# Kernel optimization log

Hardware: AMD Instinct MI355X
Metric: run time of the kernel (lower is better)

The kernel has to match this reference:

```python
import jax, jax.numpy as jnp
import numpy as np

HEADS = 16
SEGS = 8


def _rotate_half(x):
    x1, x2 = jnp.split(x, 2, axis=-1)
    return jnp.concatenate([-x2, x1], axis=-1)


def _split_heads(t, h):
    b, n, dim = t.shape
    d = dim // h
    return t.reshape(b, n, h, d).transpose(0, 2, 1, 3).reshape(b * h, n, d)


def _merge_heads(t, b, h):
    c, n, d = t.shape
    return t.reshape(b, h, n, d).transpose(0, 2, 1, 3).reshape(b, n, h * d)


def setup_inputs() -> dict:
    key = jax.random.key(0)
    ks = jax.random.split(key, 5)
    b, n, dim = 2, 4096, 1024
    x = jax.random.normal(ks[0], (b, n, dim), dtype=jnp.float32)
    w = lambda k: jax.random.normal(k, (dim, dim), dtype=jnp.float32) * 0.02
    return {
        'x': x,
        'Wq': w(ks[1]),
        'Wkv': w(ks[2]),
        'Wo': w(ks[3]),
        'bo': jnp.zeros((dim,), jnp.float32),
        'Wo0': w(ks[4]),
        'bo0': jnp.zeros((dim,), jnp.float32),
    }


def reference(x, Wq, Wkv, Wo, bo, Wo0, bo0):
    b, n, dim = x.shape
    h = HEADS
    d = dim // h
    s = SEGS
    m = n // s  # segment_len
    mask_value = -jnp.finfo(x.dtype).max

    q = _split_heads(x @ Wq, h)    # (b*h, n, d)
    kv = _split_heads(x @ Wkv, h)  # (b*h, n, d)  (serves as both keys and values)

    # rotary embedding (layer_num == 0 branch)
    inv_freq = 1.0 / (10000.0 ** (jnp.arange(0, d, 2, dtype=jnp.float32) / d))
    freqs = jnp.arange(n, dtype=jnp.float32)[:, None] * inv_freq[None, :]  # (n, d/2)
    rot = jnp.concatenate([freqs, freqs], axis=-1)[None]  # (1, n, d)
    cos, sin = jnp.cos(rot), jnp.sin(rot)
    q = q * cos + _rotate_half(q) * sin
    kv = kv * cos + _rotate_half(kv) * sin

    q = q * (d ** -0.5)

    qs = q.reshape(-1, s, m, d)   # (c, s, m, d)
    kvs = kv.reshape(-1, s, m, d)

    # overlapping windows: segment t paired with segment t+1 as kv context
    kvs_ccs = jnp.concatenate([kvs[:, :-1], kvs[:, 1:]], axis=2)  # (c, s-1, 2m, d)
    qs_ccs = qs[:, 1:]                                            # (c, s-1, m, d)

    # NOTE: original computes lkv = LayerNorm(kvs_ccs) but never uses it (dead code) -> omitted.

    lsim = jnp.einsum('csmd,csnd->csmn', qs_ccs, kvs_ccs)  # (c, s-1, m, 2m)
    causal = jnp.triu(jnp.ones((m, m), dtype=bool), 1)
    # causal mask only applied to second half of keys (the own segment t+1)
    lsim = jnp.concatenate(
        [lsim[..., :m], jnp.where(causal, mask_value, lsim[..., m:])], axis=-1)

    attn0 = jnp.einsum('csmd,csnd->csmn', qs[:, :1], kvs[:, :1])  # (c, 1, m, m)
    attn0 = jnp.where(causal, mask_value, attn0)

    attn0 = jax.nn.softmax(attn0, axis=-1)
    attn1 = jax.nn.softmax(lsim, axis=-1)

    out0 = jnp.einsum('csij,csjd->csid', attn0, kvs[:, :1]).reshape(-1, m, d)
    out1 = jnp.einsum('csij,csjd->csid', attn1, kvs_ccs).reshape(-1, (s - 1) * m, d)

    out0 = _merge_heads(out0, b, h) @ Wo0 + bo0  # (b, m, dim)
    out1 = _merge_heads(out1, b, h) @ Wo + bo    # (b, (s-1)*m, dim)
    return jnp.concatenate([out0, out1], axis=1)  # (b, n, dim)
```

## Files before the change

kernel.cpp:

```cpp
#include <hip/hip_runtime.h>
#include <hip/hip_bf16.h>
#include <float.h>

using bf16 = __hip_bfloat16;
typedef __attribute__((ext_vector_type(8))) short bf16x8;
typedef __attribute__((ext_vector_type(4))) float f32x4;
typedef __attribute__((ext_vector_type(16))) float f32x16;

#define DIM   1024
#define NSEQ  4096
#define BATCH 2
#define NH    16
#define HD    64
#define NSEG  8
#define MSEG  512
#define ROWS  (BATCH*NSEQ)
#define NC    (BATCH*NH)
#define QSCALE (0.125f * 1.44269504f)

__device__ __forceinline__ float fast_exp2(float x) {
    float r;
    asm volatile("v_exp_f32 %0, %1" : "=v"(r) : "v"(x));
    return r;
}

__device__ __forceinline__ void gload16(const bf16* g, bf16* l) {
    __builtin_amdgcn_global_load_lds((const __attribute__((address_space(1))) unsigned int*)g,
                                     (__attribute__((address_space(3))) unsigned int*)l, 16, 0, 0);
}

__global__ void k_rope_tab(float* __restrict__ cosT, float* __restrict__ sinT) {
    int idx = blockIdx.x * 256 + threadIdx.x;
    int t = idx >> 5, i = idx & 31;
    float freq = 1.0f / powf(10000.0f, (float)(2 * i) * (1.0f / 64.0f));
    float a = (float)t * freq;
    cosT[idx] = cosf(a);
    sinT[idx] = sinf(a);
}

__global__ void k_convert_x(const float* __restrict__ X, bf16* __restrict__ Xb) {
    int i = (blockIdx.x * 256 + threadIdx.x) * 4;
    float4 v = *(const float4*)&X[i];
    union { bf16 h[4]; uint2 u; } p;
    p.h[0] = __float2bfloat16(v.x);
    p.h[1] = __float2bfloat16(v.y);
    p.h[2] = __float2bfloat16(v.z);
    p.h[3] = __float2bfloat16(v.w);
    *(uint2*)&Xb[i] = p.u;
}

__global__ void k_transpose(const float* __restrict__ W, bf16* __restrict__ Wt) {
    __shared__ float tile[32][33];
    int bx = blockIdx.x * 32;
    int by = blockIdx.y * 32;
    int tx = threadIdx.x;
    for (int i = threadIdx.y; i < 32; i += 8)
        tile[i][tx] = W[(size_t)(by + i) * DIM + bx + tx];
    __syncthreads();
    for (int i = threadIdx.y; i < 32; i += 8)
        Wt[(size_t)(bx + i) * DIM + by + tx] = __float2bfloat16(tile[tx][i]);
}

__launch_bounds__(256, 4)
__global__ void k_gemm_qkv(const bf16* __restrict__ A, const bf16* __restrict__ Bq,
                           const bf16* __restrict__ Bkv, const float* __restrict__ cosT,
                           const float* __restrict__ sinT, bf16* __restrict__ Qb,
                           bf16* __restrict__ KVf) {
    __shared__ alignas(16) bf16 SH[18432];
    bf16* AsB = SH;
    bf16* BsB = SH + 8192;
    const int K = DIM;
    int tid = threadIdx.x;
    int lane = tid & 63, wave = tid >> 6;
    int hi = lane >> 5, lq = lane & 31;
    int wr = (wave >> 1) * 64, wc = (wave & 1) * 64;
    int id = blockIdx.x;
    int xcd = id & 7, rank = id >> 3;
    int by = xcd * 8 + (rank >> 4);
    int bxx = rank & 15;
    int m0 = by * 128;
    bool isQ = (bxx < 8);
    const bf16* Bt = isQ ? Bq : Bkv;
    int n0 = (bxx & 7) * 128;
    int row = lane & 15, kk = (lane >> 4) * 8;
    int ch0 = wave * 128 + lane, ch1 = ch0 + 64;
    int r0 = ch0 >> 2, c0e = (ch0 & 3) * 8;
    int r1 = ch1 >> 2, c1e = (ch1 & 3) * 8;
    f32x4 acc[4][4] = {};
    gload16(&A[(size_t)(m0 + r0) * K + c0e], &AsB[wave * 1024]);
    gload16(&A[(size_t)(m0 + r1) * K + c1e], &AsB[wave * 1024 + 512]);
    gload16(&Bt[(size_t)(n0 + r0) * K + c0e], &BsB[wave * 1024]);
    gload16(&Bt[(size_t)(n0 + r1) * K + c1e], &BsB[wave * 1024 + 512]);
    __syncthreads();
    int cur = 0;
    for (int k0 = 0; k0 < K; k0 += 32) {
        int nxt = cur ^ 1;
        if (k0 + 32 < K) {
            gload16(&A[(size_t)(m0 + r0) * K + k0 + 32 + c0e], &AsB[nxt * 4096 + wave * 1024]);
            gload16(&A[(size_t)(m0 + r1) * K + k0 + 32 + c1e], &AsB[nxt * 4096 + wave * 1024 + 512]);
            gload16(&Bt[(size_t)(n0 + r0) * K + k0 + 32 + c0e], &BsB[nxt * 4096 + wave * 1024]);
            gload16(&Bt[(size_t)(n0 + r1) * K + k0 + 32 + c1e], &BsB[nxt * 4096 + wave * 1024 + 512]);
        }
        bf16x8 af[4], bfr[4];
#pragma unroll
        for (int mt = 0; mt < 4; ++mt) af[mt] = *(const bf16x8*)&AsB[cur * 4096 + (wr + mt * 16 + row) * 32 + kk];
#pragma unroll
        for (int nt = 0; nt < 4; ++nt) bfr[nt] = *(const bf16x8*)&BsB[cur * 4096 + (wc + nt * 16 + row) * 32 + kk];
#pragma unroll
        for (int mt = 0; mt < 4; ++mt)
#pragma unroll
            for (int nt = 0; nt < 4; ++nt)
                acc[mt][nt] = __builtin_amdgcn_mfma_f32_16x16x32_bf16(af[mt], bfr[nt], acc[mt][nt], 0, 0, 0);
        __syncthreads();
        cur = nxt;
    }
    bf16* Tw = SH + wave * (64 * 72);
    int orow = (lane >> 4) * 4, ocol = lane & 15;
    int head_g = (n0 + wc) >> 6;
    float sc = isQ ? QSCALE : 1.0f;
    int bidx = (m0 + wr) >> 12;
    int tbase = (m0 + wr) & (NSEQ - 1);
    int cch = bidx * NH + head_g;
#pragma unroll
    for (int mt = 0; mt < 4; ++mt) {
#pragma unroll
        for (int i = 0; i < 4; ++i) {
            int rl = mt * 16 + orow + i;
            int t = tbase + rl;
#pragma unroll
            for (int nt = 0; nt < 2; ++nt) {
                int e = nt * 16 + ocol;
                float x1 = acc[mt][nt][i], x2 = acc[mt][nt + 2][i];
                float cv = cosT[t * 32 + e], sv = sinT[t * 32 + e];
                Tw[rl * 72 + e]      = __float2bfloat16((x1 * cv - x2 * sv) * sc);
                Tw[rl * 72 + e + 32] = __float2bfloat16((x2 * cv + x1 * sv) * sc);
            }
        }
    }
    if (isQ) {
        int rsub = lane >> 3, dg = (lane & 7) * 8;
        size_t qbase = ((size_t)cch * NSEQ + tbase) * HD;
#pragma unroll
        for (int rr = 0; rr < 8; ++rr) {
            int rl = rr * 8 + rsub;
            *(uint4*)&Qb[qbase + (size_t)rl * HD + dg] = *(const uint4*)&Tw[rl * 72 + dg];
        }
    } else {
        size_t kvfbase = ((size_t)cch * 128 + (tbase >> 5)) * 4096;
#pragma unroll
        for (int st = 0; st < 2; ++st) {
            size_t tb = kvfbase + (size_t)st * 4096;
#pragma unroll
            for (int f = 0; f < 4; ++f)
                *(uint4*)&KVf[tb + f * 512 + lane * 8] =
                    *(const uint4*)&Tw[(st * 32 + lq) * 72 + f * 16 + hi * 8];
#pragma unroll
            for (int m = 0; m < 4; ++m) {
                int d0 = (m >> 1) * 32, sb = m & 1;
                union { bf16 h[8]; uint4 u; } pk;
#pragma unroll
                for (int j = 0; j < 8; ++j)
                    pk.h[j] = Tw[(st * 32 + sb * 16 + hi * 8 + j) * 72 + d0 + lq];
                *(uint4*)&KVf[tb + (size_t)(4 + m) * 512 + lane * 8] = pk.u;
            }
        }
    }
}

__launch_bounds__(256, 4)
__global__ void k_gemm_out(const bf16* __restrict__ A, const bf16* __restrict__ Bt0,
                           const bf16* __restrict__ Bt1, const float* __restrict__ bias0,
                           const float* __restrict__ bias1, float* __restrict__ C) {
    __shared__ alignas(16) bf16 As[2][128 * 32];
    __shared__ alignas(16) bf16 Bs[2][64 * 32];
    const int K = DIM;
    int tid = threadIdx.x;
    int lane = tid & 63, wave = tid >> 6;
    int wr = (wave >> 1) * 64, wc = (wave & 1) * 32;
    int id = blockIdx.x;
    int xcd = id & 7, rank = id >> 3;
    int by = xcd * 8 + (rank >> 4);
    int bx = rank & 15;
    int m0 = by * 128, n0 = bx * 64;
    bool first = (m0 & (NSEQ - 1)) < MSEG;
    const bf16* Bt = first ? Bt0 : Bt1;
    const float* bias = first ? bias0 : bias1;
    int row = lane & 15, kk = (lane >> 4) * 8;
    int ch0 = wave * 128 + lane, ch1 = ch0 + 64;
    int r0 = ch0 >> 2, c0e = (ch0 & 3) * 8;
    int r1 = ch1 >> 2, c1e = (ch1 & 3) * 8;
    int cb = wave * 64 + lane;
    int rb = cb >> 2, cbe = (cb & 3) * 8;
    f32x4 acc[4][2] = {};
    gload16(&A[(size_t)(m0 + r0) * K + c0e], &As[0][wave * 1024]);
    gload16(&A[(size_t)(m0 + r1) * K + c1e], &As[0][wave * 1024 + 512]);
    gload16(&Bt[(size_t)(n0 + rb) * K + cbe], &Bs[0][wave * 512]);
    __syncthreads();
    int cur = 0;
    for (int k0 = 0; k0 < K; k0 += 32) {
        int nxt = cur ^ 1;
        if (k0 + 32 < K) {
            gload16(&A[(size_t)(m0 + r0) * K + k0 + 32 + c0e], &As[nxt][wave * 1024]);
            gload16(&A[(size_t)(m0 + r1) * K + k0 + 32 + c1e], &As[nxt][wave * 1024 + 512]);
            gload16(&Bt[(size_t)(n0 + rb) * K + k0 + 32 + cbe], &Bs[nxt][wave * 512]);
        }
        bf16x8 af[4], bfr[2];
#pragma unroll
        for (int mt = 0; mt < 4; ++mt) af[mt] = *(const bf16x8*)&As[cur][(wr + mt * 16 + row) * 32 + kk];
#pragma unroll
        for (int nt = 0; nt < 2; ++nt) bfr[nt] = *(const bf16x8*)&Bs[cur][(wc + nt * 16 + row) * 32 + kk];
#pragma unroll
        for (int mt = 0; mt < 4; ++mt)
#pragma unroll
            for (int nt = 0; nt < 2; ++nt)
                acc[mt][nt] = __builtin_amdgcn_mfma_f32_16x16x32_bf16(af[mt], bfr[nt], acc[mt][nt], 0, 0, 0);
        __syncthreads();
        cur = nxt;
    }
    int orow = (lane >> 4) * 4, ocol = lane & 15;
#pragma unroll
    for (int mt = 0; mt < 4; ++mt)
#pragma unroll
        for (int nt = 0; nt < 2; ++nt) {
            float bv = bias[n0 + wc + nt * 16 + ocol];
#pragma unroll
            for (int i = 0; i < 4; ++i)
                C[(size_t)(m0 + wr + mt * 16 + orow + i) * DIM + n0 + wc + nt * 16 + ocol] = acc[mt][nt][i] + bv;
        }
}

__launch_bounds__(256, 4)
__global__ void k_attn(const bf16* __restrict__ Qb, const bf16* __restrict__ KVf,
                       bf16* __restrict__ Ob) {
    int lane = threadIdx.x & 63, wave = threadIdx.x >> 6;
    int hi = lane >> 5, lq = lane & 31;
    int id = blockIdx.x;
    int xcd = id & 7, rank = id >> 3;
    int c = xcd * 4 + (rank & 3);
    int hr = rank >> 2;
    int bx, seg;
    if (hr < 28) { bx = 3 - hr / 7; seg = 1 + hr % 7; }
    else         { seg = 0; bx = 31 - hr; }
    int i0 = bx * 128 + wave * 32;
    int bidx = c >> 4, head = c & 15;
    int tq = seg * MSEG + i0 + lq;
    const bf16* qptr = &Qb[((size_t)c * NSEQ + tq) * HD + hi * 8];
    bf16x8 qf[4];
#pragma unroll
    for (int dc = 0; dc < 4; ++dc) qf[dc] = *(const bf16x8*)&qptr[dc * 16];
    f32x16 o0 = {}, o1 = {};
    float mrun = -FLT_MAX, lrun = 0.f;
    int kvbase = (seg == 0) ? 0 : (seg - 1) * MSEG;
    int cstart = (seg == 0) ? 0 : MSEG;
    int cend = cstart + i0 + 32;
    int nT = cend >> 5;

    const bf16* fb = &KVf[((size_t)c * 128 + (kvbase >> 5)) * 4096 + lane * 8];

    bf16x8 ka0, ka1, ka2, ka3;
    f32x16 s;
    {
        bf16x8 k0 = *(const bf16x8*)&fb[0];
        bf16x8 k1 = *(const bf16x8*)&fb[512];
        bf16x8 k2 = *(const bf16x8*)&fb[1024];
        bf16x8 k3 = *(const bf16x8*)&fb[1536];
        if (nT > 1) {
            const bf16* p1 = fb + 4096;
            ka0 = *(const bf16x8*)&p1[0];
            ka1 = *(const bf16x8*)&p1[512];
            ka2 = *(const bf16x8*)&p1[1024];
            ka3 = *(const bf16x8*)&p1[1536];
        }
        f32x16 z = {};
        __builtin_amdgcn_s_setprio(1);
        z = __builtin_amdgcn_mfma_f32_32x32x16_bf16(k0, qf[0], z, 0, 0, 0);
        z = __builtin_amdgcn_mfma_f32_32x32x16_bf16(k1, qf[1], z, 0, 0, 0);
        z = __builtin_amdgcn_mfma_f32_32x32x16_bf16(k2, qf[2], z, 0, 0, 0);
        z = __builtin_amdgcn_mfma_f32_32x32x16_bf16(k3, qf[3], z, 0, 0, 0);
        __builtin_amdgcn_s_setprio(0);
        s = z;
    }

    for (int it = 0; it < nT; ++it) {
        int c0 = it * 32;
        const bf16* pv = fb + (size_t)it * 4096 + 2048;
        bf16x8 vf0 = *(const bf16x8*)&pv[0];
        bf16x8 vf1 = *(const bf16x8*)&pv[512];
        bf16x8 vf2 = *(const bf16x8*)&pv[1024];
        bf16x8 vf3 = *(const bf16x8*)&pv[1536];
        if (c0 + 31 >= cstart && c0 + 31 - cstart > i0) {
#pragma unroll
            for (int r = 0; r < 16; ++r) {
                int kvg = c0 + ((r & 3) + 8 * (r >> 2) + 4 * hi);
                if (kvg >= cstart && kvg - cstart > i0 + lq) s[r] = -FLT_MAX;
            }
        }
        float m8[8], m4[4];
#pragma unroll
        for (int r = 0; r < 8; ++r) m8[r] = fmaxf(s[2 * r], s[2 * r + 1]);
#pragma unroll
        for (int r = 0; r < 4; ++r) m4[r] = fmaxf(m8[2 * r], m8[2 * r + 1]);
        float vmax = fmaxf(fmaxf(m4[0], m4[1]), fmaxf(m4[2], m4[3]));
        vmax = fmaxf(vmax, __shfl_xor(vmax, 32));
        if (__any(vmax > mrun + 11.5f)) {
            float nm = fmaxf(mrun, vmax);
            float al = fast_exp2(mrun - nm);
#pragma unroll
            for (int r = 0; r < 16; ++r) { o0[r] *= al; o1[r] *= al; }
            lrun *= al;
            mrun = nm;
        }
        float p[16];
#pragma unroll
        for (int r = 0; r < 16; ++r) p[r] = fast_exp2(s[r] - mrun);
        if (it + 1 < nT) {
            f32x16 z = {};
            __builtin_amdgcn_s_setprio(1);
            z = __builtin_amdgcn_mfma_f32_32x32x16_bf16(ka0, qf[0], z, 0, 0, 0);
            z = __builtin_amdgcn_mfma_f32_32x32x16_bf16(ka1, qf[1], z, 0, 0, 0);
            z = __builtin_amdgcn_mfma_f32_32x32x16_bf16(ka2, qf[2], z, 0, 0, 0);
            z = __builtin_amdgcn_mfma_f32_32x32x16_bf16(ka3, qf[3], z, 0, 0, 0);
            __builtin_amdgcn_s_setprio(0);
            s = z;
            if (it + 2 < nT) {
                const bf16* pn = fb + (size_t)(it + 2) * 4096;
                ka0 = *(const bf16x8*)&pn[0];
                ka1 = *(const bf16x8*)&pn[512];
                ka2 = *(const bf16x8*)&pn[1024];
                ka3 = *(const bf16x8*)&pn[1536];
            }
        }
        float a8[8], a4[4];
#pragma unroll
        for (int r = 0; r < 8; ++r) a8[r] = p[2 * r] + p[2 * r + 1];
#pragma unroll
        for (int r = 0; r < 4; ++r) a4[r] = a8[2 * r] + a8[2 * r + 1];
        lrun += (a4[0] + a4[1]) + (a4[2] + a4[3]);
        unsigned pk[8];
#pragma unroll
        for (int k = 0; k < 8; ++k) {
            union { bf16 h[2]; unsigned u; } cv;
            cv.h[0] = __float2bfloat16(p[2 * k]);
            cv.h[1] = __float2bfloat16(p[2 * k + 1]);
            pk[k] = cv.u;
        }
        unsigned u0 = hi ? pk[0] : pk[2];
        unsigned u1 = hi ? pk[1] : pk[3];
        unsigned u2 = hi ? pk[4] : pk[6];
        unsigned u3 = hi ? pk[5] : pk[7];
        unsigned w0 = (unsigned)__shfl_xor((int)u0, 32);
        unsigned w1 = (unsigned)__shfl_xor((int)u1, 32);
        unsigned w2 = (unsigned)__shfl_xor((int)u2, 32);
        unsigned w3 = (unsigned)__shfl_xor((int)u3, 32);
        union { unsigned u[4]; bf16x8 v; } b0, b1;
        b0.u[0] = hi ? w0 : pk[0];
        b0.u[1] = hi ? w1 : pk[1];
        b0.u[2] = hi ? pk[2] : w0;
        b0.u[3] = hi ? pk[3] : w1;
        b1.u[0] = hi ? w2 : pk[4];
        b1.u[1] = hi ? w3 : pk[5];
        b1.u[2] = hi ? pk[6] : w2;
        b1.u[3] = hi ? pk[7] : w3;
        __builtin_amdgcn_s_setprio(1);
        o0 = __builtin_amdgcn_mfma_f32_32x32x16_bf16(vf0, b0.v, o0, 0, 0, 0);
        o1 = __builtin_amdgcn_mfma_f32_32x32x16_bf16(vf2, b0.v, o1, 0, 0, 0);
        o0 = __builtin_amdgcn_mfma_f32_32x32x16_bf16(vf1, b1.v, o0, 0, 0, 0);
        o1 = __builtin_amdgcn_mfma_f32_32x32x16_bf16(vf3, b1.v, o1, 0, 0, 0);
        __builtin_amdgcn_s_setprio(0);
    }
    lrun += __shfl_xor(lrun, 32);
    float inv = 1.0f / lrun;
    size_t obase = ((size_t)bidx * NSEQ + tq) * DIM + head * HD;
#pragma unroll
    for (int dt = 0; dt < 2; ++dt)
#pragma unroll
        for (int a = 0; a < 4; ++a) {
            union { bf16 h[4]; uint2 u; } pkd;
            const f32x16& ov = dt ? o1 : o0;
#pragma unroll
            for (int i = 0; i < 4; ++i) pkd.h[i] = __float2bfloat16(ov[4 * a + i] * inv);
            *(uint2*)&Ob[obase + dt * 32 + 8 * a + 4 * hi] = pkd.u;
        }
}

extern "C" void kernel_launch(void* const* d_in, const int* in_sizes, int n_in,
                              void* d_out, int out_size, void* d_ws, size_t ws_size,
                              hipStream_t stream) {
    const float* x   = (const float*)d_in[0];
    const float* Wq  = (const float*)d_in[1];
    const float* Wkv = (const float*)d_in[2];
    const float* Wo  = (const float*)d_in[3];
    const float* bo  = (const float*)d_in[4];
    const float* Wo0 = (const float*)d_in[5];
    const float* bo0 = (const float*)d_in[6];
    float* out = (float*)d_out;

    char* ws = (char*)d_ws;
    size_t off = 0;
    auto alloc = [&](size_t bytes) { void* p = ws + off; off += (bytes + 255) & ~(size_t)255; return p; };
    float* cosT = (float*)alloc((size_t)NSEQ * 32 * 4);
    float* sinT = (float*)alloc((size_t)NSEQ * 32 * 4);
    bf16* Xb    = (bf16*)alloc((size_t)ROWS * DIM * 2);
    bf16* WqT   = (bf16*)alloc((size_t)DIM * DIM * 2);
    bf16* WkvT  = (bf16*)alloc((size_t)DIM * DIM * 2);
    bf16* WoT   = (bf16*)alloc((size_t)DIM * DIM * 2);
    bf16* Wo0T  = (bf16*)alloc((size_t)DIM * DIM * 2);
    bf16* Qb    = (bf16*)alloc((size_t)NC * NSEQ * HD * 2);
    bf16* KVf   = (bf16*)alloc((size_t)NC * 128 * 4096 * 2);
    bf16* Ob    = (bf16*)alloc((size_t)ROWS * DIM * 2);

    hipLaunchKernelGGL(k_rope_tab, dim3(NSEQ * 32 / 256), dim3(256), 0, stream, cosT, sinT);
    hipLaunchKernelGGL(k_convert_x, dim3(ROWS * DIM / 4 / 256), dim3(256), 0, stream, x, Xb);
    hipLaunchKernelGGL(k_transpose, dim3(32, 32), dim3(32, 8), 0, stream, Wq, WqT);
    hipLaunchKernelGGL(k_transpose, dim3(32, 32), dim3(32, 8), 0, stream, Wkv, WkvT);
    hipLaunchKernelGGL(k_transpose, dim3(32, 32), dim3(32, 8), 0, stream, Wo, WoT);
    hipLaunchKernelGGL(k_transpose, dim3(32, 32), dim3(32, 8), 0, stream, Wo0, Wo0T);

    hipLaunchKernelGGL(k_gemm_qkv, dim3(1024), dim3(256), 0, stream, Xb, WqT, WkvT, cosT, sinT, Qb, KVf);

    hipLaunchKernelGGL(k_attn, dim3(1024), dim3(256), 0, stream, Qb, KVf, Ob);

    hipLaunchKernelGGL(k_gemm_out, dim3(1024), dim3(256), 0, stream, Ob, Wo0T, WoT, bo0, bo, out);
}
```

Measured before the change: 158.2 us.

## Triple-buffer LDS staging in QKV and output GEMMs with partial vmcnt waits

```diff
diff --git a/kernel.cpp b/kernel.cpp
--- a/kernel.cpp
+++ b/kernel.cpp
@@ -61,14 +61,14 @@
         Wt[(size_t)(bx + i) * DIM + by + tx] = __float2bfloat16(tile[tx][i]);
 }
 
-__launch_bounds__(256, 4)
+__launch_bounds__(256, 3)
 __global__ void k_gemm_qkv(const bf16* __restrict__ A, const bf16* __restrict__ Bq,
                            const bf16* __restrict__ Bkv, const float* __restrict__ cosT,
                            const float* __restrict__ sinT, bf16* __restrict__ Qb,
                            bf16* __restrict__ KVf) {
-    __shared__ alignas(16) bf16 SH[18432];
+    __shared__ alignas(16) bf16 SH[24576];
     bf16* AsB = SH;
-    bf16* BsB = SH + 8192;
+    bf16* BsB = SH + 12288;
     const int K = DIM;
     int tid = threadIdx.x;
     int lane = tid & 63, wave = tid >> 6;
@@ -87,19 +87,23 @@
     int r0 = ch0 >> 2, c0e = (ch0 & 3) * 8;
     int r1 = ch1 >> 2, c1e = (ch1 & 3) * 8;
     f32x4 acc[4][4] = {};
-    gload16(&A[(size_t)(m0 + r0) * K + c0e], &AsB[wave * 1024]);
-    gload16(&A[(size_t)(m0 + r1) * K + c1e], &AsB[wave * 1024 + 512]);
-    gload16(&Bt[(size_t)(n0 + r0) * K + c0e], &BsB[wave * 1024]);
-    gload16(&Bt[(size_t)(n0 + r1) * K + c1e], &BsB[wave * 1024 + 512]);
-    __syncthreads();
+
+    auto stage = [&](int k0, int b) {
+        gload16(&A[(size_t)(m0 + r0) * K + k0 + c0e], &AsB[b * 4096 + wave * 1024]);
+        gload16(&A[(size_t)(m0 + r1) * K + k0 + c1e], &AsB[b * 4096 + wave * 1024 + 512]);
+        gload16(&Bt[(size_t)(n0 + r0) * K + k0 + c0e], &BsB[b * 4096 + wave * 1024]);
+        gload16(&Bt[(size_t)(n0 + r1) * K + k0 + c1e], &BsB[b * 4096 + wave * 1024 + 512]);
+    };
+    stage(0, 0);
+    stage(32, 1);
+    asm volatile("s_waitcnt vmcnt(4)" ::: "memory");
+    __builtin_amdgcn_s_barrier();
+    __builtin_amdgcn_sched_barrier(0);
     int cur = 0;
-    for (int k0 = 0; k0 < K; k0 += 32) {
-        int nxt = cur ^ 1;
-        if (k0 + 32 < K) {
-            gload16(&A[(size_t)(m0 + r0) * K + k0 + 32 + c0e], &AsB[nxt * 4096 + wave * 1024]);
-            gload16(&A[(size_t)(m0 + r1) * K + k0 + 32 + c1e], &AsB[nxt * 4096 + wave * 1024 + 512]);
-            gload16(&Bt[(size_t)(n0 + r0) * K + k0 + 32 + c0e], &BsB[nxt * 4096 + wave * 1024]);
-            gload16(&Bt[(size_t)(n0 + r1) * K + k0 + 32 + c1e], &BsB[nxt * 4096 + wave * 1024 + 512]);
+    for (int k = 0; k < 32; ++k) {
+        if (k + 2 < 32) {
+            int nb = cur + 2; if (nb >= 3) nb -= 3;
+            stage(k * 32 + 64, nb);
         }
         bf16x8 af[4], bfr[4];
 #pragma unroll
@@ -111,9 +115,15 @@
 #pragma unroll
             for (int nt = 0; nt < 4; ++nt)
                 acc[mt][nt] = __builtin_amdgcn_mfma_f32_16x16x32_bf16(af[mt], bfr[nt], acc[mt][nt], 0, 0, 0);
-        __syncthreads();
-        cur = nxt;
-    }
+        if (k + 1 < 32) {
+            if (k + 2 < 32) asm volatile("s_waitcnt vmcnt(4)" ::: "memory");
+            else            asm volatile("s_waitcnt vmcnt(0)" ::: "memory");
+            __builtin_amdgcn_s_barrier();
+            __builtin_amdgcn_sched_barrier(0);
+        }
+        cur = cur + 1; if (cur == 3) cur = 0;
+    }
+    __syncthreads();
     bf16* Tw = SH + wave * (64 * 72);
     int orow = (lane >> 4) * 4, ocol = lane & 15;
     int head_g = (n0 + wc) >> 6;
@@ -171,8 +181,8 @@
 __global__ void k_gemm_out(const bf16* __restrict__ A, const bf16* __restrict__ Bt0,
                            const bf16* __restrict__ Bt1, const float* __restrict__ bias0,
                            const float* __restrict__ bias1, float* __restrict__ C) {
-    __shared__ alignas(16) bf16 As[2][128 * 32];
-    __shared__ alignas(16) bf16 Bs[2][64 * 32];
+    __shared__ alignas(16) bf16 As[3][128 * 32];
+    __shared__ alignas(16) bf16 Bs[3][64 * 32];
     const int K = DIM;
     int tid = threadIdx.x;
     int lane = tid & 63, wave = tid >> 6;
@@ -192,17 +202,22 @@
     int cb = wave * 64 + lane;
     int rb = cb >> 2, cbe = (cb & 3) * 8;
     f32x4 acc[4][2] = {};
-    gload16(&A[(size_t)(m0 + r0) * K + c0e], &As[0][wave * 1024]);
-    gload16(&A[(size_t)(m0 + r1) * K + c1e], &As[0][wave * 1024 + 512]);
-    gload16(&Bt[(size_t)(n0 + rb) * K + cbe], &Bs[0][wave * 512]);
-    __syncthreads();
+
+    auto stage = [&](int k0, int b) {
+        gload16(&A[(size_t)(m0 + r0) * K + k0 + c0e], &As[b][wave * 1024]);
+        gload16(&A[(size_t)(m0 + r1) * K + k0 + c1e], &As[b][wave * 1024 + 512]);
+        gload16(&Bt[(size_t)(n0 + rb) * K + k0 + cbe], &Bs[b][wave * 512]);
+    };
+    stage(0, 0);
+    stage(32, 1);
+    asm volatile("s_waitcnt vmcnt(3)" ::: "memory");
+    __builtin_amdgcn_s_barrier();
+    __builtin_amdgcn_sched_barrier(0);
     int cur = 0;
-    for (int k0 = 0; k0 < K; k0 += 32) {
-        int nxt = cur ^ 1;
-        if (k0 + 32 < K) {
-            gload16(&A[(size_t)(m0 + r0) * K + k0 + 32 + c0e], &As[nxt][wave * 1024]);
-            gload16(&A[(size_t)(m0 + r1) * K + k0 + 32 + c1e], &As[nxt][wave * 1024 + 512]);
-            gload16(&Bt[(size_t)(n0 + rb) * K + k0 + 32 + cbe], &Bs[nxt][wave * 512]);
+    for (int k = 0; k < 32; ++k) {
+        if (k + 2 < 32) {
+            int nb = cur + 2; if (nb >= 3) nb -= 3;
+            stage(k * 32 + 64, nb);
         }
         bf16x8 af[4], bfr[2];
 #pragma unroll
@@ -214,8 +229,13 @@
 #pragma unroll
             for (int nt = 0; nt < 2; ++nt)
                 acc[mt][nt] = __builtin_amdgcn_mfma_f32_16x16x32_bf16(af[mt], bfr[nt], acc[mt][nt], 0, 0, 0);
-        __syncthreads();
-        cur = nxt;
+        if (k + 1 < 32) {
+            if (k + 2 < 32) asm volatile("s_waitcnt vmcnt(3)" ::: "memory");
+            else            asm volatile("s_waitcnt vmcnt(0)" ::: "memory");
+            __builtin_amdgcn_s_barrier();
+            __builtin_amdgcn_sched_barrier(0);
+        }
+        cur = cur + 1; if (cur == 3) cur = 0;
     }
     int orow = (lane >> 4) * 4, ocol = lane & 15;
 #pragma unroll
```

Result: faster. 154.5 us (-2.4%).
